# Optimization experiments

Hardware: AMD Instinct MI355X
Metric: run time of the kernel (lower is better)

The kernel has to match this reference:

```python
import jax, jax.numpy as jnp
import numpy as np

SXY_BF, SC_BF = 70.0, 12.0
COMPAT_BF, COMPAT_SPATIAL = 4.0, 2.0
SXY_SPATIAL = 6
NUM_ITER = 5
N_OUT = 21


def _gkern_depthwise(std, chans):
    # matches gkern(): sig_sq even -> r = sig_sq - 1, s = 2r+1
    sig_sq = std ** 2
    r = sig_sq if sig_sq % 2 else sig_sq - 1
    s = 2 * r + 1
    yy, xx = np.meshgrid(np.arange(s), np.arange(s), indexing='ij')
    k = np.exp(-(((yy - r) ** 2 + (xx - r) ** 2) / (2.0 * sig_sq)))
    k = k / k.sum()
    # original builds a [C,C,s,s] diagonal kernel == depthwise [C,1,s,s]
    return jnp.asarray(np.broadcast_to(k[None, None], (chans, 1, s, s)).copy(), jnp.float32)


def setup_inputs() -> dict:
    key = jax.random.key(0)
    k1, k2 = jax.random.split(key)
    unary = jax.random.uniform(k1, (2, N_OUT, 64, 64), dtype=jnp.float32)
    ref = jax.random.uniform(k2, (2, 3, 64, 64), dtype=jnp.float32) * 255.0  # RGB image
    gk = _gkern_depthwise(SXY_SPATIAL, N_OUT)
    kstd = jnp.asarray([SXY_BF, SXY_BF, SC_BF, SC_BF, SC_BF], jnp.float32)
    return {"unary": unary, "ref": ref, "gk": gk, "kstd": kstd}


def _crf_forward(unary, ref, gk, kstd):
    N, C, H, W = unary.shape
    P = H * W
    # stacked reference features: [y, x, r, g, b]
    yy, xx = jnp.meshgrid(jnp.arange(H, dtype=jnp.float32),
                          jnp.arange(W, dtype=jnp.float32), indexing='ij')
    grid = jnp.broadcast_to(jnp.stack([yy, xx])[None], (N, 2, H, W))
    stacked = jnp.concatenate([grid, ref], axis=1)  # [N,5,H,W]
    feats = (stacked / kstd[None, :, None, None]).reshape(N, -1, P).transpose(0, 2, 1)  # [N,P,5]
    # exact dense Gaussian (bilateral) kernel: K[p,q] = exp(-||f_p - f_q||^2 / 2)
    sq = jnp.sum(feats * feats, axis=-1)  # [N,P]
    d2 = sq[:, :, None] + sq[:, None, :] - 2.0 * jnp.einsum('npd,nqd->npq', feats, feats)
    K = jnp.exp(-0.5 * jnp.maximum(d2, 0.0))  # [N,P,P]

    U = jnp.log(jnp.clip(unary, 1e-5, 1.0))
    q = jax.nn.softmax(U, axis=1)
    pad = gk.shape[-1] // 2
    for i in range(NUM_ITER):
        qbf = jnp.einsum('npq,ncq->ncp', K, q.reshape(N, C, P)).reshape(N, C, H, W)
        qsf = jax.lax.conv_general_dilated(
            q, gk, window_strides=(1, 1), padding=[(pad, pad), (pad, pad)],
            feature_group_count=C, dimension_numbers=('NCHW', 'OIHW', 'NCHW'))
        q_hat = U + COMPAT_BF * qbf + COMPAT_SPATIAL * qsf
        q = jax.nn.softmax(q_hat, axis=1)  # normalize_final_iter=True
    return q


def reference(unary, ref, gk, kstd):
    return _crf_forward(unary, ref, gk, kstd)
```

## Files before the change

### kernel.cpp

```cpp
#include <hip/hip_runtime.h>
#include <math.h>

#ifndef __has_builtin
#define __has_builtin(x) 0
#endif
#if __has_builtin(__builtin_amdgcn_exp2f)
#define EXP2F(x) __builtin_amdgcn_exp2f(x)
#else
#define EXP2F(x) exp2f(x)
#endif

#define L2E  1.44269504088896340736f
#define RL2E 0.69314718055994530942f

#define NBATCH 2
#define NC 21
#define NP 4096
#define KR 35
#define KS 71

typedef _Float16 half_t;
typedef _Float16 h8 __attribute__((ext_vector_type(8)));
typedef _Float16 h4 __attribute__((ext_vector_type(4)));
typedef float f4 __attribute__((ext_vector_type(4)));
typedef float f2 __attribute__((ext_vector_type(2)));
#define MFMA16(a, b, c) __builtin_amdgcn_mfma_f32_16x16x32_f16((a), (b), (c), 0, 0, 0)

static __device__ __forceinline__ f2 pk_fma(f2 a, f2 b, f2 c) {
    f2 d;
    asm volatile("v_pk_fma_f32 %0, %1, %2, %3" : "=v"(d) : "v"(a), "v"(b), "v"(c));
    return d;
}
static __device__ __forceinline__ f2 pk_add(f2 a, f2 b) {
    f2 d;
    asm volatile("v_pk_add_f32 %0, %1, %2" : "=v"(d) : "v"(a), "v"(b));
    return d;
}

#define PTILE 128
#define NPT   32
#define SQ    16
#define CHUNK 256
#define STEPS 8
#define NBBIL (NBATCH * NPT * SQ)
#define NBCONV (NBATCH * NC)
#define SEGS_PER_S 1024
#define SEG_HALVES 256

#define OFF_QFEAT 0
#define OFF_QSOA  65536
#define OFF_UT    114688
#define OFF_QSF   311296
#define OFF_G     483328
#define OFF_QH16  485376
#define OFF_PART  845824

#define LDS_BYTES 27648
#define QLS_STRIDE 264

__global__ __launch_bounds__(256) void setup_kernel(
    const float* __restrict__ unary, const float* __restrict__ ref,
    const float* __restrict__ kstd, float* __restrict__ ws,
    float* __restrict__ outq)
{
    int gid = blockIdx.x * 256 + threadIdx.x;
    if (gid < 4096) {
        float s = 0.f;
        for (int t = -KR; t <= KR; ++t) s += expf(-(float)(t * t) * (1.0f / 72.0f));
        int y = gid >> 6, yp = gid & 63;
        int d = y - yp;
        float v = (d >= -KR && d <= KR) ? expf(-(float)(d * d) * (1.0f / 72.0f)) / s : 0.f;
        ((half_t*)(ws + OFF_G))[gid] = (half_t)v;
    }
    if (gid >= NBATCH * NP) return;
    int n = gid >> 12, p = gid & (NP - 1);
    int y = p >> 6, x = p & 63;
    float k0 = kstd[0], k1 = kstd[1], k2 = kstd[2], k3 = kstd[3], k4 = kstd[4];
    const float* rp = ref + n * 3 * NP + p;
    float f0 = (float)y / k0;
    float f1 = (float)x / k1;
    float f2_ = rp[0]      / k2;
    float f3 = rp[NP]     / k3;
    float f4_ = rp[2 * NP] / k4;
    float sq = f0*f0 + f1*f1 + f2_*f2_ + f3*f3 + f4_*f4_;
    float h  = -0.5f * L2E * sq;
    float* qf = ws + OFF_QFEAT + gid * 8;
    qf[0]=L2E*f0; qf[1]=L2E*f1; qf[2]=L2E*f2_; qf[3]=L2E*f3; qf[4]=L2E*f4_;
    qf[5]=h; qf[6]=0.f; qf[7]=0.f;
    float* qs = ws + OFF_QSOA;
    qs[0*8192 + gid] = L2E*f0;  qs[1*8192 + gid] = L2E*f1;
    qs[2*8192 + gid] = L2E*f2_; qs[3*8192 + gid] = L2E*f3;
    qs[4*8192 + gid] = L2E*f4_; qs[5*8192 + gid] = h;

    float U[NC], e[NC];
    const float* up = unary + n * NC * NP + p;
    float m = -1e30f;
    for (int c = 0; c < NC; ++c) {
        float u = up[c * NP];
        u = fminf(fmaxf(u, 1e-5f), 1.0f);
        U[c] = logf(u);
        m = fmaxf(m, U[c]);
    }
    float ssum = 0.f;
    for (int c = 0; c < NC; ++c) { e[c] = EXP2F(L2E * (U[c] - m)); ssum += e[c]; }
    float inv = 1.0f / ssum;
    float* ut = ws + OFF_UT + gid * 24;
    half_t* qh = (half_t*)(ws + OFF_QH16);
    for (int c = 0; c < NC; ++c) {
        float qv = e[c] * inv;
        ut[c] = U[c];
        qh[(n * 24 + c) * NP + p] = (half_t)qv;
        outq[(n * NC + c) * NP + p] = qv;
    }
    ut[21] = 0.f; ut[22] = 0.f; ut[23] = 0.f;
    qh[(n * 24 + 21) * NP + p] = (half_t)0.f;
    qh[(n * 24 + 22) * NP + p] = (half_t)0.f;
    qh[(n * 24 + 23) * NP + p] = (half_t)0.f;
}

__global__ __launch_bounds__(256) void bilat_conv_kernel(
    const float* __restrict__ qfeatA,
    const float* __restrict__ qsoa,
    const half_t* __restrict__ qh16,
    const half_t* __restrict__ gmat,
    half_t* __restrict__ part,
    float* __restrict__ qsf)
{
    __shared__ __align__(16) char lds[LDS_BYTES];
    int b = blockIdx.x;
    int tid = threadIdx.x;
    int l = tid & 63, w = tid >> 6;

    if (b < NBBIL) {
        int n  = b & 1;
        int pt = (b >> 1) & (NPT - 1);
        int s  = b >> 6;
        float*  qsoaS = (float*)lds;
        half_t* qls   = (half_t*)(lds + 6144);

        for (int i = tid; i < 6 * (CHUNK / 4); i += 256) {
            int d = i >> 6, g = i & 63;
            *(f4*)(qsoaS + d * CHUNK + g * 4) =
                *(const f4*)(qsoa + (size_t)d * 8192 + n * NP + s * CHUNK + g * 4);
        }
        for (int i = tid; i < 21 * (CHUNK / 8); i += 256) {
            int c = i >> 5, g = i & 31;
            *(h8*)(qls + c * QLS_STRIDE + g * 8) =
                *(const h8*)(qh16 + (size_t)(n * 24 + c) * NP + s * CHUNK + g * 8);
        }
        for (int i = tid; i < 11 * 33; i += 256) {
            int c = 21 + i / 33, g = i % 33;
            *(h8*)(qls + c * QLS_STRIDE + g * 8) = (h8)(half_t)0.f;
        }
        f2 pf2[2][5], ph2[2];
        #pragma unroll
        for (int mt = 0; mt < 2; ++mt) {
            const float* fp = qfeatA + (size_t)(n * NP + pt * PTILE + (w * 2 + mt) * 16 + (l & 15)) * 8;
            #pragma unroll
            for (int i = 0; i < 5; ++i) {
                float v = fp[i] * RL2E;
                pf2[mt][i] = (f2){v, v};
            }
            ph2[mt] = (f2){fp[5], fp[5]};
        }
        f4 acc[2][2];
        #pragma unroll
        for (int mt = 0; mt < 2; ++mt) { acc[mt][0] = (f4)0.f; acc[mt][1] = (f4)0.f; }
        int kq = (l >> 4) * 8;
        __syncthreads();

        for (int step = 0; step < STEPS; ++step) {
            int qbase = step * 32 + kq;
            h8 kv[2];
            #pragma unroll
            for (int hf = 0; hf < 2; ++hf) {
                f4 qf0 = *(const f4*)(qsoaS + 0 * CHUNK + qbase + hf * 4);
                f4 qf1 = *(const f4*)(qsoaS + 1 * CHUNK + qbase + hf * 4);
                f4 qf2 = *(const f4*)(qsoaS + 2 * CHUNK + qbase + hf * 4);
                f4 qf3 = *(const f4*)(qsoaS + 3 * CHUNK + qbase + hf * 4);
                f4 qf4 = *(const f4*)(qsoaS + 4 * CHUNK + qbase + hf * 4);
                f4 qf5 = *(const f4*)(qsoaS + 5 * CHUNK + qbase + hf * 4);
                #pragma unroll
                for (int pr = 0; pr < 2; ++pr) {
                    f2 q0 = {qf0[2*pr], qf0[2*pr+1]};
                    f2 q1 = {qf1[2*pr], qf1[2*pr+1]};
                    f2 q2 = {qf2[2*pr], qf2[2*pr+1]};
                    f2 q3 = {qf3[2*pr], qf3[2*pr+1]};
                    f2 q4 = {qf4[2*pr], qf4[2*pr+1]};
                    f2 qh2 = {qf5[2*pr], qf5[2*pr+1]};
                    #pragma unroll
                    for (int mt = 0; mt < 2; ++mt) {
                        f2 e = pk_add(qh2, ph2[mt]);
                        e = pk_fma(pf2[mt][0], q0, e);
                        e = pk_fma(pf2[mt][1], q1, e);
                        e = pk_fma(pf2[mt][2], q2, e);
                        e = pk_fma(pf2[mt][3], q3, e);
                        e = pk_fma(pf2[mt][4], q4, e);
                        kv[mt][hf * 4 + pr * 2]     = (half_t)EXP2F(e[0]);
                        kv[mt][hf * 4 + pr * 2 + 1] = (half_t)EXP2F(e[1]);
                    }
                }
            }
            h8 bf0 = *(const h8*)(qls + (size_t)(l & 15) * QLS_STRIDE + qbase);
            h8 bf1 = *(const h8*)(qls + (size_t)(16 + (l & 15)) * QLS_STRIDE + qbase);
            #pragma unroll
            for (int mt = 0; mt < 2; ++mt) {
                acc[mt][0] = MFMA16(kv[mt], bf0, acc[mt][0]);
                acc[mt][1] = MFMA16(kv[mt], bf1, acc[mt][1]);
            }
        }
        #pragma unroll
        for (int mt = 0; mt < 2; ++mt) {
            #pragma unroll
            for (int cht = 0; cht < 2; ++cht) {
                int segFlat = ((((s * 2 + n) * NPT + pt) * 4 + w) * 2 + mt) * 2 + cht;
                h4 hv;
                hv[0] = (half_t)acc[mt][cht][0];
                hv[1] = (half_t)acc[mt][cht][1];
                hv[2] = (half_t)acc[mt][cht][2];
                hv[3] = (half_t)acc[mt][cht][3];
                *(h4*)(part + (size_t)segFlat * SEG_HALVES + l * 4) = hv;
            }
        }
    } else {
        int cb = b - NBBIL;
        int n = cb / NC, c = cb % NC;
        half_t* qt = (half_t*)lds;
        half_t* gl = (half_t*)(lds + 9216);
        half_t* dl = (half_t*)(lds + 18432);

        for (int i = tid; i < 512; i += 256) {
            int row = i >> 3, g = i & 7;
            *(h8*)(gl + row * 72 + g * 8) = *(const h8*)(gmat + row * 64 + g * 8);
        }
        const half_t* qsrc = qh16 + (size_t)(n * 24 + c) * NP;
        for (int i = tid; i < 512; i += 256) {
            int row = i >> 3, g = i & 7;
            h8 v = *(const h8*)(qsrc + row * 64 + g * 8);
            #pragma unroll
            for (int k = 0; k < 8; ++k) qt[(g * 8 + k) * 72 + row] = v[k];
        }
        __syncthreads();

        int m0 = w * 16;
        f4 acc1[4];
        #pragma unroll
        for (int nt = 0; nt < 4; ++nt) acc1[nt] = (f4)0.f;
        #pragma unroll
        for (int ks = 0; ks < 2; ++ks) {
            h8 af = *(const h8*)(gl + (size_t)(m0 + (l & 15)) * 72 + ks * 32 + (l >> 4) * 8);
            #pragma unroll
            for (int nt = 0; nt < 4; ++nt) {
                h8 bf = *(const h8*)(qt + (size_t)(nt * 16 + (l & 15)) * 72 + ks * 32 + (l >> 4) * 8);
                acc1[nt] = MFMA16(af, bf, acc1[nt]);
            }
        }
        #pragma unroll
        for (int nt = 0; nt < 4; ++nt)
            #pragma unroll
            for (int r = 0; r < 4; ++r)
                dl[(size_t)(m0 + (l >> 4) * 4 + r) * 72 + nt * 16 + (l & 15)] = (half_t)acc1[nt][r];
        __syncthreads();

        f4 acc2[4];
        #pragma unroll
        for (int nt = 0; nt < 4; ++nt) acc2[nt] = (f4)0.f;
        #pragma unroll
        for (int ks = 0; ks < 2; ++ks) {
            h8 af = *(const h8*)(dl + (size_t)(m0 + (l & 15)) * 72 + ks * 32 + (l >> 4) * 8);
            #pragma unroll
            for (int nt = 0; nt < 4; ++nt) {
                h8 bf = *(const h8*)(gl + (size_t)(nt * 16 + (l & 15)) * 72 + ks * 32 + (l >> 4) * 8);
                acc2[nt] = MFMA16(af, bf, acc2[nt]);
            }
        }
        float* dst = qsf + (size_t)(n * NC + c) * NP;
        #pragma unroll
        for (int nt = 0; nt < 4; ++nt)
            #pragma unroll
            for (int r = 0; r < 4; ++r)
                dst[(size_t)(m0 + (l >> 4) * 4 + r) * 64 + nt * 16 + (l & 15)] = acc2[nt][r];
    }
}

__global__ __launch_bounds__(256) void reduce_update_kernel(
    const half_t* __restrict__ part, const float* __restrict__ ut_,
    const float* __restrict__ qsf, float* __restrict__ outq,
    half_t* __restrict__ qh16)
{
    __shared__ float red[4096];
    int rb = blockIdx.x;
    int tid = threadIdx.x;
    int n = rb & 1, pt = rb >> 1;

    float acc[16];
    #pragma unroll
    for (int k = 0; k < 16; ++k) acc[k] = 0.f;
    for (int s = 0; s < SQ; ++s) {
        size_t base = (size_t)(((s * 2 + n) * NPT + pt) * 16) * SEG_HALVES;
        #pragma unroll
        for (int k = 0; k < 4; ++k) {
            h4 v = *(const h4*)(part + base + (size_t)(k * 256 + tid) * 4);
            acc[k*4+0] += (float)v[0]; acc[k*4+1] += (float)v[1];
            acc[k*4+2] += (float)v[2]; acc[k*4+3] += (float)v[3];
        }
    }
    #pragma unroll
    for (int k = 0; k < 4; ++k)
        *(f4*)(red + (k * 256 + tid) * 4) =
            (f4){acc[k*4+0], acc[k*4+1], acc[k*4+2], acc[k*4+3]};
    __syncthreads();

    if (tid < PTILE) {
        int pp = tid;
        int p = pt * PTILE + pp;
        int gid = n * NP + p;
        int mt_g = pp >> 4;
        int wv = mt_g >> 1, mtl = mt_g & 1;
        int mrow = pp & 15;
        int lg = mrow >> 2, reg = mrow & 3;
        int segL = wv * 4 + mtl * 2;

        float lg_[NC], e[NC];
        const float* ut = ut_ + (size_t)gid * 24;
        const float* qs = qsf + (size_t)n * NC * NP + p;
        float m = -1e30f;
        #pragma unroll
        for (int c = 0; c < NC; ++c) {
            int cht = c >> 4, chL = c & 15;
            float qb = red[(segL + cht) * 256 + (lg * 16 + chL) * 4 + reg];
            float li = ut[c] + 4.0f * qb + 2.0f * qs[c * NP];
            lg_[c] = li;
            m = fmaxf(m, li);
        }
        float ssum = 0.f;
        #pragma unroll
        for (int c = 0; c < NC; ++c) { e[c] = EXP2F(L2E * (lg_[c] - m)); ssum += e[c]; }
        float inv = 1.0f / ssum;
        #pragma unroll
        for (int c = 0; c < NC; ++c) {
            float qv = e[c] * inv;
            outq[(size_t)(n * NC + c) * NP + p] = qv;
            qh16[(size_t)(n * 24 + c) * NP + p] = (half_t)qv;
        }
    }
}

extern "C" void kernel_launch(void* const* d_in, const int* in_sizes, int n_in,
                              void* d_out, int out_size, void* d_ws, size_t ws_size,
                              hipStream_t stream)
{
    const float* unary = (const float*)d_in[0];
    const float* ref   = (const float*)d_in[1];
    const float* kstd  = (const float*)d_in[3];
    float* ws   = (float*)d_ws;
    float* outq = (float*)d_out;

    const float*  qfeatA = ws + OFF_QFEAT;
    const float*  qsoa   = ws + OFF_QSOA;
    float*        ut     = ws + OFF_UT;
    float*        qsf    = ws + OFF_QSF;
    const half_t* gmat   = (const half_t*)(ws + OFF_G);
    half_t*       qh16   = (half_t*)(ws + OFF_QH16);
    half_t*       part   = (half_t*)(ws + OFF_PART);

    setup_kernel<<<32, 256, 0, stream>>>(unary, ref, kstd, ws, outq);
    for (int it = 0; it < 5; ++it) {
        bilat_conv_kernel<<<NBBIL + NBCONV, 256, 0, stream>>>(
            qfeatA, qsoa, qh16, gmat, part, qsf);
        reduce_update_kernel<<<64, 256, 0, stream>>>(part, ut, qsf, outq, qh16);
    }
}
```

Before: 155.6 us.

## Materialize bilateral kernel matrix once in fp16 and reuse across iterations

New measurement: 169.5 us. 8.9% more time.

```diff
diff --git a/kernel.cpp b/kernel.cpp
--- a/kernel.cpp
+++ b/kernel.cpp
@@ -54,6 +54,7 @@
 #define OFF_G     483328
 #define OFF_QH16  485376
 #define OFF_PART  845824
+#define OFF_KF    2942976
 
 #define LDS_BYTES 27648
 #define QLS_STRIDE 264
@@ -118,13 +119,77 @@
     qh[(n * 24 + 23) * NP + p] = (half_t)0.f;
 }
 
+static __device__ __forceinline__ void conv_body(
+    char* lds, int cb, int tid, int l, int w,
+    const half_t* __restrict__ qh16, const half_t* __restrict__ gmat,
+    float* __restrict__ qsf)
+{
+    int n = cb / NC, c = cb % NC;
+    half_t* qt = (half_t*)lds;
+    half_t* gl = (half_t*)(lds + 9216);
+    half_t* dl = (half_t*)(lds + 18432);
+
+    for (int i = tid; i < 512; i += 256) {
+        int row = i >> 3, g = i & 7;
+        *(h8*)(gl + row * 72 + g * 8) = *(const h8*)(gmat + row * 64 + g * 8);
+    }
+    const half_t* qsrc = qh16 + (size_t)(n * 24 + c) * NP;
+    for (int i = tid; i < 512; i += 256) {
+        int row = i >> 3, g = i & 7;
+        h8 v = *(const h8*)(qsrc + row * 64 + g * 8);
+        #pragma unroll
+        for (int k = 0; k < 8; ++k) qt[(g * 8 + k) * 72 + row] = v[k];
+    }
+    __syncthreads();
+
+    int m0 = w * 16;
+    f4 acc1[4];
+    #pragma unroll
+    for (int nt = 0; nt < 4; ++nt) acc1[nt] = (f4)0.f;
+    #pragma unroll
+    for (int ks = 0; ks < 2; ++ks) {
+        h8 af = *(const h8*)(gl + (size_t)(m0 + (l & 15)) * 72 + ks * 32 + (l >> 4) * 8);
+        #pragma unroll
+        for (int nt = 0; nt < 4; ++nt) {
+            h8 bf = *(const h8*)(qt + (size_t)(nt * 16 + (l & 15)) * 72 + ks * 32 + (l >> 4) * 8);
+            acc1[nt] = MFMA16(af, bf, acc1[nt]);
+        }
+    }
+    #pragma unroll
+    for (int nt = 0; nt < 4; ++nt)
+        #pragma unroll
+        for (int r = 0; r < 4; ++r)
+            dl[(size_t)(m0 + (l >> 4) * 4 + r) * 72 + nt * 16 + (l & 15)] = (half_t)acc1[nt][r];
+    __syncthreads();
+
+    f4 acc2[4];
+    #pragma unroll
+    for (int nt = 0; nt < 4; ++nt) acc2[nt] = (f4)0.f;
+    #pragma unroll
+    for (int ks = 0; ks < 2; ++ks) {
+        h8 af = *(const h8*)(dl + (size_t)(m0 + (l & 15)) * 72 + ks * 32 + (l >> 4) * 8);
+        #pragma unroll
+        for (int nt = 0; nt < 4; ++nt) {
+            h8 bf = *(const h8*)(gl + (size_t)(nt * 16 + (l & 15)) * 72 + ks * 32 + (l >> 4) * 8);
+            acc2[nt] = MFMA16(af, bf, acc2[nt]);
+        }
+    }
+    float* dst = qsf + (size_t)(n * NC + c) * NP;
+    #pragma unroll
+    for (int nt = 0; nt < 4; ++nt)
+        #pragma unroll
+        for (int r = 0; r < 4; ++r)
+            dst[(size_t)(m0 + (l >> 4) * 4 + r) * 64 + nt * 16 + (l & 15)] = acc2[nt][r];
+}
+
 __global__ __launch_bounds__(256) void bilat_conv_kernel(
     const float* __restrict__ qfeatA,
     const float* __restrict__ qsoa,
     const half_t* __restrict__ qh16,
     const half_t* __restrict__ gmat,
     half_t* __restrict__ part,
-    float* __restrict__ qsf)
+    float* __restrict__ qsf,
+    half_t* __restrict__ kf)
 {
     __shared__ __align__(16) char lds[LDS_BYTES];
     int b = blockIdx.x;
@@ -201,6 +266,12 @@
                     }
                 }
             }
+            int qstep = s * STEPS + step;
+            #pragma unroll
+            for (int mt = 0; mt < 2; ++mt) {
+                int pt16 = pt * 8 + w * 2 + mt;
+                *(h8*)(kf + ((size_t)(n * 256 + pt16) * 128 + qstep) * 512 + l * 8) = kv[mt];
+            }
             h8 bf0 = *(const h8*)(qls + (size_t)(l & 15) * QLS_STRIDE + qbase);
             h8 bf1 = *(const h8*)(qls + (size_t)(16 + (l & 15)) * QLS_STRIDE + qbase);
             #pragma unroll
@@ -223,63 +294,77 @@
             }
         }
     } else {
-        int cb = b - NBBIL;
-        int n = cb / NC, c = cb % NC;
-        half_t* qt = (half_t*)lds;
-        half_t* gl = (half_t*)(lds + 9216);
-        half_t* dl = (half_t*)(lds + 18432);
-
-        for (int i = tid; i < 512; i += 256) {
-            int row = i >> 3, g = i & 7;
-            *(h8*)(gl + row * 72 + g * 8) = *(const h8*)(gmat + row * 64 + g * 8);
-        }
-        const half_t* qsrc = qh16 + (size_t)(n * 24 + c) * NP;
-        for (int i = tid; i < 512; i += 256) {
-            int row = i >> 3, g = i & 7;
-            h8 v = *(const h8*)(qsrc + row * 64 + g * 8);
-            #pragma unroll
-            for (int k = 0; k < 8; ++k) qt[(g * 8 + k) * 72 + row] = v[k];
-        }
+        conv_body(lds, b - NBBIL, tid, l, w, qh16, gmat, qsf);
+    }
+}
+
+__global__ __launch_bounds__(256) void gemm_conv_kernel(
+    const half_t* __restrict__ kf,
+    const half_t* __restrict__ qh16,
+    const half_t* __restrict__ gmat,
+    half_t* __restrict__ part,
+    float* __restrict__ qsf)
+{
+    __shared__ __align__(16) char lds[LDS_BYTES];
+    int b = blockIdx.x;
+    int tid = threadIdx.x;
+    int l = tid & 63, w = tid >> 6;
+
+    if (b < NBBIL) {
+        int n  = b & 1;
+        int pt = (b >> 1) & (NPT - 1);
+        int s  = b >> 6;
+        half_t* qls = (half_t*)lds;
+
+        for (int i = tid; i < 21 * (CHUNK / 8); i += 256) {
+            int c = i >> 5, g = i & 31;
+            *(h8*)(qls + c * QLS_STRIDE + g * 8) =
+                *(const h8*)(qh16 + (size_t)(n * 24 + c) * NP + s * CHUNK + g * 8);
+        }
+        for (int i = tid; i < 11 * 33; i += 256) {
+            int c = 21 + i / 33, g = i % 33;
+            *(h8*)(qls + c * QLS_STRIDE + g * 8) = (h8)(half_t)0.f;
+        }
+        f4 acc[2][2];
+        #pragma unroll
+        for (int mt = 0; mt < 2; ++mt) { acc[mt][0] = (f4)0.f; acc[mt][1] = (f4)0.f; }
+        int kq = (l >> 4) * 8;
+        int pt16b = pt * 8 + w * 2;
+        const half_t* kf0 = kf + ((size_t)(n * 256 + pt16b) * 128 + s * STEPS) * 512 + l * 8;
+        const half_t* kf1 = kf0 + (size_t)128 * 512;
         __syncthreads();
 
-        int m0 = w * 16;
-        f4 acc1[4];
-        #pragma unroll
-        for (int nt = 0; nt < 4; ++nt) acc1[nt] = (f4)0.f;
-        #pragma unroll
-        for (int ks = 0; ks < 2; ++ks) {
-            h8 af = *(const h8*)(gl + (size_t)(m0 + (l & 15)) * 72 + ks * 32 + (l >> 4) * 8);
-            #pragma unroll
-            for (int nt = 0; nt < 4; ++nt) {
-                h8 bf = *(const h8*)(qt + (size_t)(nt * 16 + (l & 15)) * 72 + ks * 32 + (l >> 4) * 8);
-                acc1[nt] = MFMA16(af, bf, acc1[nt]);
-            }
-        }
-        #pragma unroll
-        for (int nt = 0; nt < 4; ++nt)
-            #pragma unroll
-            for (int r = 0; r < 4; ++r)
-                dl[(size_t)(m0 + (l >> 4) * 4 + r) * 72 + nt * 16 + (l & 15)] = (half_t)acc1[nt][r];
-        __syncthreads();
-
-        f4 acc2[4];
-        #pragma unroll
-        for (int nt = 0; nt < 4; ++nt) acc2[nt] = (f4)0.f;
-        #pragma unroll
-        for (int ks = 0; ks < 2; ++ks) {
-            h8 af = *(const h8*)(dl + (size_t)(m0 + (l & 15)) * 72 + ks * 32 + (l >> 4) * 8);
-            #pragma unroll
-            for (int nt = 0; nt < 4; ++nt) {
-                h8 bf = *(const h8*)(gl + (size_t)(nt * 16 + (l & 15)) * 72 + ks * 32 + (l >> 4) * 8);
-                acc2[nt] = MFMA16(af, bf, acc2[nt]);
-            }
-        }
-        float* dst = qsf + (size_t)(n * NC + c) * NP;
-        #pragma unroll
-        for (int nt = 0; nt < 4; ++nt)
-            #pragma unroll
-            for (int r = 0; r < 4; ++r)
-                dst[(size_t)(m0 + (l >> 4) * 4 + r) * 64 + nt * 16 + (l & 15)] = acc2[nt][r];
+        h8 av0 = *(const h8*)(kf0);
+        h8 av1 = *(const h8*)(kf1);
+        for (int step = 0; step < STEPS; ++step) {
+            int qbase = step * 32 + kq;
+            h8 cur0 = av0, cur1 = av1;
+            if (step < STEPS - 1) {
+                av0 = *(const h8*)(kf0 + (size_t)(step + 1) * 512);
+                av1 = *(const h8*)(kf1 + (size_t)(step + 1) * 512);
+            }
+            h8 bf0 = *(const h8*)(qls + (size_t)(l & 15) * QLS_STRIDE + qbase);
+            h8 bf1 = *(const h8*)(qls + (size_t)(16 + (l & 15)) * QLS_STRIDE + qbase);
+            acc[0][0] = MFMA16(cur0, bf0, acc[0][0]);
+            acc[0][1] = MFMA16(cur0, bf1, acc[0][1]);
+            acc[1][0] = MFMA16(cur1, bf0, acc[1][0]);
+            acc[1][1] = MFMA16(cur1, bf1, acc[1][1]);
+        }
+        #pragma unroll
+        for (int mt = 0; mt < 2; ++mt) {
+            #pragma unroll
+            for (int cht = 0; cht < 2; ++cht) {
+                int segFlat = ((((s * 2 + n) * NPT + pt) * 4 + w) * 2 + mt) * 2 + cht;
+                h4 hv;
+                hv[0] = (half_t)acc[mt][cht][0];
+                hv[1] = (half_t)acc[mt][cht][1];
+                hv[2] = (half_t)acc[mt][cht][2];
+                hv[3] = (half_t)acc[mt][cht][3];
+                *(h4*)(part + (size_t)segFlat * SEG_HALVES + l * 4) = hv;
+            }
+        }
+    } else {
+        conv_body(lds, b - NBBIL, tid, l, w, qh16, gmat, qsf);
     }
 }
 
@@ -363,11 +448,15 @@
     const half_t* gmat   = (const half_t*)(ws + OFF_G);
     half_t*       qh16   = (half_t*)(ws + OFF_QH16);
     half_t*       part   = (half_t*)(ws + OFF_PART);
+    half_t*       kf     = (half_t*)(ws + OFF_KF);
 
     setup_kernel<<<32, 256, 0, stream>>>(unary, ref, kstd, ws, outq);
-    for (int it = 0; it < 5; ++it) {
-        bilat_conv_kernel<<<NBBIL + NBCONV, 256, 0, stream>>>(
-            qfeatA, qsoa, qh16, gmat, part, qsf);
+    bilat_conv_kernel<<<NBBIL + NBCONV, 256, 0, stream>>>(
+        qfeatA, qsoa, qh16, gmat, part, qsf, kf);
+    reduce_update_kernel<<<64, 256, 0, stream>>>(part, ut, qsf, outq, qh16);
+    for (int it = 1; it < 5; ++it) {
+        gemm_conv_kernel<<<NBBIL + NBCONV, 256, 0, stream>>>(
+            kf, qh16, gmat, part, qsf);
         reduce_update_kernel<<<64, 256, 0, stream>>>(part, ut, qsf, outq, qh16);
     }
 }
```
